# Performance work log

Measured on AMD Instinct MI355X. Metric: run time of the kernel, lower is better.

## Reference

```python
import jax, jax.numpy as jnp
import numpy as np

NB_STEPS = 50
ALPHA = 0.9
NUM_RNN_STEPS = 2
B = 4096
NUM_FEATURE = 100
IN_D = 5
HIDDEN = [64, 64, 64]
P1 = (1.1, 1.1, 1.5, 2.0, 2.5)   # IntegrandNN_outer_level powers
P2 = (1.5, 2.0, 2.5, 3.0, 3.5)   # IntegrandNN powers


def _cc(nb_steps):
    # Clenshaw-Curtis weights/steps, identical to UMNN's compute_cc_weights
    n = nb_steps
    i = np.arange(n + 1, dtype=np.float64).reshape(-1, 1)
    lam = np.cos(i @ i.T * np.pi / n)
    lam[:, 0] = 0.5
    lam[:, -1] *= 0.5
    lam = lam * 2.0 / n
    W = np.zeros(n + 1)
    even = np.arange(0, n + 1, 2)
    W[even] = 2.0 / (1.0 - even.astype(np.float64) ** 2)
    W[0] = 1.0
    ccw = (lam.T @ W).astype(np.float32)                         # [n+1]
    steps = np.cos(np.arange(n + 1) * np.pi / n).astype(np.float32)  # [n+1]
    return jnp.asarray(ccw), jnp.asarray(steps)

CC_W, CC_S = _cc(NB_STEPS)


def _mlp(xh, Ws, bs):
    # Linear+ReLU stack with ELU on the last layer (ReLU popped, ELU appended)
    h = xh
    for W, b in zip(Ws[:-1], bs[:-1]):
        h = jax.nn.relu(h @ W.T + b)
    return jax.nn.elu(h @ Ws[-1].T + bs[-1])


def _integrand(x, h, Ws, bs, Wf, powers):
    z = _mlp(jnp.concatenate([x, h], axis=1), Ws, bs) + 1.0      # [N,1], z >= 0
    feats = jnp.concatenate([z ** p for p in powers], axis=1)    # [N,5]
    return jax.nn.relu((1.0 / (feats + 1.0)) @ Wf.T)             # [N,1]


def _integrate(x0, xT, h, f):
    # ParallelNeuralIntegral forward: CC quadrature of f from x0 to xT
    Bn, S = x0.shape[0], NB_STEPS + 1
    X = x0[:, None, :] + (xT - x0)[:, None, :] * (CC_S[None, :, None] + 1.0) / 2.0  # [B,S,1]
    hs = jnp.broadcast_to(h[:, None, :], (Bn, S, h.shape[1])).reshape(-1, h.shape[1])
    dz = f(X.reshape(-1, 1), hs).reshape(Bn, S, 1)
    return (dz * CC_W[None, :, None]).sum(1) * (xT - x0) / 2.0   # [B,1]


def setup_inputs() -> dict:
    key = jax.random.key(0)
    ks = jax.random.split(key, 24)
    def lin(k, o, i):
        return jax.random.normal(k, (o, i), jnp.float32) / np.sqrt(i)
    d = {}
    d["x_"] = jax.random.normal(ks[0], (B, NUM_FEATURE), jnp.float32)
    d["h_"] = jax.random.normal(ks[1], (B, IN_D - 1), jnp.float32)
    d["log_weight"] = jnp.ones((1, NUM_FEATURE), jnp.float32)     # reset_parameters -> 1
    d["sigmoid_param"] = jnp.zeros((1,), jnp.float32)
    sizes = [IN_D] + HIDDEN + [1]
    for tag, base in (("f1", 2), ("f2", 12)):
        for li, (i, o) in enumerate(zip(sizes[:-1], sizes[1:])):
            d[f"{tag}_W{li}"] = lin(ks[base + 2 * li], o, i)
            d[f"{tag}_b{li}"] = jnp.zeros((o,), jnp.float32)
        d[f"{tag}_Wf"] = jnp.abs(lin(ks[base + 9], 1, 5))         # reset_params -> abs
    return d


def reference(x_, h_, log_weight, sigmoid_param,
              f1_W0, f1_b0, f1_W1, f1_b1, f1_W2, f1_b2, f1_W3, f1_b3, f1_Wf,
              f2_W0, f2_b0, f2_W1, f2_b1, f2_W2, f2_b2, f2_W3, f2_b3, f2_Wf):
    f1Ws = [f1_W0, f1_W1, f1_W2, f1_W3]; f1bs = [f1_b0, f1_b1, f1_b2, f1_b3]
    f2Ws = [f2_W0, f2_W1, f2_W2, f2_W3]; f2bs = [f2_b0, f2_b1, f2_b2, f2_b3]
    f1 = lambda x, h: _integrand(x, h, f1Ws, f1bs, f1_Wf, P1)
    f2 = lambda x, h: _integrand(x, h, f2Ws, f2bs, f2_Wf, P2)

    # modular function: linear to [B,1] then sum over dim 1 -> [B,1]
    xm = jnp.sum(x_ * log_weight[0], axis=1, keepdims=True)
    lam = jax.nn.sigmoid(sigmoid_param[0])

    I1 = jnp.zeros_like(xm)
    I2 = jnp.zeros_like(xm)
    out_first = None
    for _ in range(NUM_RNN_STEPS):
        x = (1.0 - lam) * xm + lam * I1
        x2 = (1.0 - lam) * xm + lam * I2
        out_first = f1(x2, h_)
        I1 = _integrate(jnp.zeros_like(x), x, h_, f1)
        xmax = jnp.max(x2) + 10.0
        xfinal = jnp.zeros_like(x) + xmax
        I2 = (1.0 / ALPHA) * _integrate(x2, xfinal, h_, f2)
    return I1, out_first, I2
```

## Files before the change

### kernel.cpp

```cpp
#include <hip/hip_runtime.h>
#include <math.h>

typedef _Float16 half8v __attribute__((ext_vector_type(8)));
typedef _Float16 half4v __attribute__((ext_vector_type(4)));
typedef _Float16 half2v __attribute__((ext_vector_type(2)));
typedef float float4v __attribute__((ext_vector_type(4)));

#define BB    4096
#define NS    51
#define INV_ALPHA (1.0f/0.9f)

#define WS_CCW   0
#define WS_CCS   64
#define WS_LAM   128
#define WS_KEY64 160
#define WS_PM    256
#define WS_XM    512
#define WS_X     (WS_XM + BB)
#define WS_X2    (WS_X + BB)
#define WS_H     16384
#define H_NET    8192
#define H_W2     4096
#define H_W0     16384
#define H_W3     20480

#if defined(__has_builtin)
#if __has_builtin(__builtin_amdgcn_rcpf)
#define FRCP(x) __builtin_amdgcn_rcpf(x)
#endif
#if __has_builtin(__builtin_amdgcn_exp2f)
#define FEXP2(x) __builtin_amdgcn_exp2f(x)
#endif
#if __has_builtin(__builtin_amdgcn_logf)
#define FLOG2(x) __builtin_amdgcn_logf(x)
#endif
#endif
#ifndef FRCP
#define FRCP(x) (1.0f / (x))
#endif
#ifndef FEXP2
#define FEXP2(x) exp2f(x)
#endif
#ifndef FLOG2
#define FLOG2(x) log2f(x)
#endif

__device__ __forceinline__ unsigned fkey(float f) {
    int i = __float_as_int(f);
    return (i >= 0) ? ((unsigned)i + 0x80000000u) : ~(unsigned)i;
}
__device__ __forceinline__ float fkey_inv(unsigned k) {
    return (k & 0x80000000u) ? __int_as_float((int)(k - 0x80000000u))
                             : __int_as_float((int)~k);
}

__device__ __forceinline__ int swz(int row, int cb) {
    return (row << 6) + (((cb ^ (row & 7)) & 7) << 3);
}

__device__ __forceinline__ half4v pk_relu4(float4v c) {
#if defined(__has_builtin) && __has_builtin(__builtin_amdgcn_cvt_pkrtz)
    half2v a = __builtin_bit_cast(half2v,
        __builtin_amdgcn_cvt_pkrtz(fmaxf(c[0], 0.0f), fmaxf(c[1], 0.0f)));
    half2v b = __builtin_bit_cast(half2v,
        __builtin_amdgcn_cvt_pkrtz(fmaxf(c[2], 0.0f), fmaxf(c[3], 0.0f)));
    half4v o; o[0] = a[0]; o[1] = a[1]; o[2] = b[0]; o[3] = b[1];
    return o;
#else
    half4v o;
    o[0] = (_Float16)fmaxf(c[0], 0.0f); o[1] = (_Float16)fmaxf(c[1], 0.0f);
    o[2] = (_Float16)fmaxf(c[2], 0.0f); o[3] = (_Float16)fmaxf(c[3], 0.0f);
    return o;
#endif
}

__global__ void k_setup(const float* __restrict__ x_, const float* __restrict__ lw,
                        const float* __restrict__ sp,
                        const float* __restrict__ f1W0, const float* __restrict__ f1W1,
                        const float* __restrict__ f1W2, const float* __restrict__ f1W3,
                        const float* __restrict__ f2W0, const float* __restrict__ f2W1,
                        const float* __restrict__ f2W2, const float* __restrict__ f2W3,
                        float* __restrict__ ws) {
    _Float16* wh = (_Float16*)(ws + WS_H);
    const int blk = blockIdx.x, tid = threadIdx.x;
    if (blk < 256) {
        int wave = tid >> 6, lane = tid & 63;
        float vmax = -1e30f;
        for (int r = 0; r < 4; ++r) {
            int row = blk * 16 + wave * 4 + r;
            float v = 0.0f;
            for (int i = lane; i < 100; i += 64) v = fmaf(x_[row * 100 + i], lw[i], v);
            #pragma unroll
            for (int off = 32; off > 0; off >>= 1) v += __shfl_xor(v, off, 64);
            if (lane == 0) ws[WS_XM + row] = v;
            vmax = fmaxf(vmax, v);
        }
        __shared__ float sm[4];
        if (lane == 0) sm[wave] = vmax;
        __syncthreads();
        if (tid == 0)
            ws[WS_PM + blk] = fmaxf(fmaxf(sm[0], sm[1]), fmaxf(sm[2], sm[3]));
    } else if (blk < 272) {
        int t = (blk - 256) * 256 + tid;
        wh[t]                = (_Float16)f1W1[t];
        wh[H_W2 + t]         = (_Float16)f1W2[t];
        wh[H_NET + t]        = (_Float16)f2W1[t];
        wh[H_NET + H_W2 + t] = (_Float16)f2W2[t];
        if (t < 2048) {
            int j = t >> 5, k = t & 31;
            wh[H_W0 + t]        = (k < 5) ? (_Float16)f1W0[j * 5 + k] : (_Float16)0.0f;
            wh[H_W0 + 2048 + t] = (k < 5) ? (_Float16)f2W0[j * 5 + k] : (_Float16)0.0f;
        }
        if (t < 64) {
            wh[H_W3 + t]      = (_Float16)f1W3[t];
            wh[H_W3 + 64 + t] = (_Float16)f2W3[t];
        }
    } else {
        if (tid < 64) ((unsigned*)ws)[WS_KEY64 + tid] = 0u;
        if (tid == 64) ws[WS_LAM] = 1.0f / (1.0f + expf(-sp[0]));
        if (tid >= 128 && tid <= 178) {
            int s = tid - 128;
            ws[WS_CCS + s] = cospif((float)s / 50.0f);
            float acc = 0.0f;
            for (int a = 0; a <= 50; ++a) {
                float w;
                if (a == 0) w = 1.0f;
                else if ((a & 1) == 0) w = 2.0f / (1.0f - (float)(a * a));
                else continue;
                float l;
                if (s == 0) l = 0.5f;
                else {
                    int m = (a * s) % 100;
                    l = cospif((float)m / 50.0f);
                    if (s == 50) l *= 0.5f;
                }
                acc += l * 0.04f * w;
            }
            ws[WS_CCW + s] = acc;
        }
    }
}

__global__ __launch_bounds__(64, 2) void k_int(
    int mode, float* __restrict__ ws, const float* __restrict__ h_,
    const float* __restrict__ f1b0, const float* __restrict__ f1b1,
    const float* __restrict__ f1b2, const float* __restrict__ f1b3,
    const float* __restrict__ f1Wf,
    const float* __restrict__ f2b0, const float* __restrict__ f2b1,
    const float* __restrict__ f2b2, const float* __restrict__ f2b3,
    const float* __restrict__ f2Wf,
    float* __restrict__ out)
{
    __shared__ _Float16 act[64 * 64];

    const int blk = blockIdx.x;
    const int lane = threadIdx.x;
    const int lo = lane & 15, q = lane >> 4;

    const float* xm = ws + WS_XM;
    const float* xarr = ws + WS_X;
    const float* x2arr = ws + WS_X2;
    const _Float16* wh = (const _Float16*)(ws + WS_H);
    const float lam = ws[WS_LAM];
    const float oml = 1.0f - lam;

    const bool u2 = (blk >= 1024);
    const int kb0 = u2 ? blk - 1024 : blk;

    const _Float16* W0h = wh + H_W0 + (u2 ? 2048 : 0);
    const _Float16* W1h = wh + (u2 ? H_NET : 0);
    const _Float16* W2h = W1h + H_W2;
    const _Float16* W3h = wh + H_W3 + (u2 ? 64 : 0);
    const float* B0 = u2 ? f2b0 : f1b0;
    const float* B1 = u2 ? f2b1 : f1b1;
    const float* B2 = u2 ? f2b2 : f1b2;
    const float* B3 = u2 ? f2b3 : f1b3;
    const float* WF = u2 ? f2Wf : f1Wf;
    const float p0 = u2 ? 1.5f : 1.1f;
    const float p1 = u2 ? 2.0f : 1.1f;
    const float p2 = u2 ? 2.5f : 1.5f;
    const float p3 = u2 ? 3.0f : 2.0f;
    const float p4 = u2 ? 3.5f : 2.5f;

    half8v A0w[4], A1w[4][2], A2w[4][2];
    float4v b0r[4], b1r[4], b2r[4];
    half4v w3r[4];
    #pragma unroll
    for (int m = 0; m < 4; ++m) {
        A0w[m]    = *(const half8v*)(W0h + (16 * m + lo) * 32 + q * 8);
        A1w[m][0] = *(const half8v*)(W1h + (16 * m + lo) * 64 + q * 8);
        A1w[m][1] = *(const half8v*)(W1h + (16 * m + lo) * 64 + 32 + q * 8);
        A2w[m][0] = *(const half8v*)(W2h + (16 * m + lo) * 64 + q * 8);
        A2w[m][1] = *(const half8v*)(W2h + (16 * m + lo) * 64 + 32 + q * 8);
        b0r[m] = *(const float4v*)(B0 + 16 * m + q * 4);
        b1r[m] = *(const float4v*)(B1 + 16 * m + q * 4);
        b2r[m] = *(const float4v*)(B2 + 16 * m + q * 4);
        w3r[m] = *(const half4v*)(W3h + 16 * m + 4 * q);
    }
    const float B3s = B3[0];
    const float wf0 = WF[0], wf1 = WF[1], wf2 = WF[2], wf3 = WF[3], wf4 = WF[4];

    float t_r[4];
    #pragma unroll
    for (int n = 0; n < 4; ++n) {
        int r = 16 * n + lo;
        t_r[n] = (ws[WS_CCS + (r > 50 ? 50 : r)] + 1.0f) * 0.5f;
    }
    const float ccw_l = (lane <= 50) ? ws[WS_CCW + lane] : 0.0f;

    float xmax = 0.0f;
    if (u2) {
        if (mode) {
            float v = fkey_inv(((const unsigned*)ws)[WS_KEY64 + lane]);
            #pragma unroll
            for (int off = 32; off > 0; off >>= 1) v = fmaxf(v, __shfl_xor(v, off, 64));
            xmax = v + 10.0f;
        } else {
            const float* pm = ws + WS_PM;
            float v = fmaxf(fmaxf(pm[lane], pm[lane + 64]),
                            fmaxf(pm[lane + 128], pm[lane + 192]));
            #pragma unroll
            for (int off = 32; off > 0; off >>= 1) v = fmaxf(v, __shfl_xor(v, off, 64));
            xmax = oml * v + 10.0f;
        }
    }

    const int nitems = (mode && !u2 && blk < 64) ? 5 : 4;

    #pragma clang loop unroll(disable)
    for (int it = 0; it < nitems; ++it) {
        const bool last = (it == 4);
        int b = kb0 + 1024 * it;
        float xb = 0.0f, x0 = 0.0f;
        float4 h4u = {0, 0, 0, 0};

        half8v Bf0[4];
        if (last) {
            int b0i = blk * 64;
            #pragma unroll
            for (int n = 0; n < 4; ++n) {
                int idx = b0i + 16 * n + lo;
                float xr = x2arr[idx];
                float4 hr = ((const float4*)h_)[idx];
                half8v e;
                e[0] = (_Float16)xr; e[1] = (_Float16)hr.x; e[2] = (_Float16)hr.y;
                e[3] = (_Float16)hr.z; e[4] = (_Float16)hr.w;
                e[5] = (_Float16)0.0f; e[6] = (_Float16)0.0f; e[7] = (_Float16)0.0f;
                half8v z;
                #pragma unroll
                for (int t2 = 0; t2 < 8; ++t2) z[t2] = (_Float16)0.0f;
                Bf0[n] = (q == 0) ? e : z;
            }
        } else {
            if (!u2) xb = mode ? xarr[b] : oml * xm[b];
            else     x0 = mode ? x2arr[b] : oml * xm[b];
            h4u = ((const float4*)h_)[b];
            #pragma unroll
            for (int n = 0; n < 4; ++n) {
                float xr = (!u2) ? xb * t_r[n] : x0 + (xmax - x0) * t_r[n];
                half8v e;
                e[0] = (_Float16)xr; e[1] = (_Float16)h4u.x; e[2] = (_Float16)h4u.y;
                e[3] = (_Float16)h4u.z; e[4] = (_Float16)h4u.w;
                e[5] = (_Float16)0.0f; e[6] = (_Float16)0.0f; e[7] = (_Float16)0.0f;
                half8v z;
                #pragma unroll
                for (int t2 = 0; t2 < 8; ++t2) z[t2] = (_Float16)0.0f;
                Bf0[n] = (q == 0) ? e : z;
            }
        }

        #pragma unroll
        for (int m = 0; m < 4; ++m)
            #pragma unroll
            for (int n = 0; n < 4; ++n) {
                float4v c = __builtin_amdgcn_mfma_f32_16x16x32_f16(A0w[m], Bf0[n], b0r[m], 0, 0, 0);
                *(half4v*)(act + swz(16 * n + lo, 2 * m + (q >> 1)) + 4 * (q & 1)) = pk_relu4(c);
            }

        {
            half8v Bf[2][4];
            #pragma unroll
            for (int kb = 0; kb < 2; ++kb)
                #pragma unroll
                for (int n = 0; n < 4; ++n)
                    Bf[kb][n] = *(const half8v*)(act + swz(16 * n + lo, 4 * kb + q));
            #pragma unroll
            for (int m = 0; m < 4; ++m)
                #pragma unroll
                for (int n = 0; n < 4; ++n) {
                    float4v c = __builtin_amdgcn_mfma_f32_16x16x32_f16(A1w[m][0], Bf[0][n], b1r[m], 0, 0, 0);
                    c = __builtin_amdgcn_mfma_f32_16x16x32_f16(A1w[m][1], Bf[1][n], c, 0, 0, 0);
                    *(half4v*)(act + swz(16 * n + lo, 2 * m + (q >> 1)) + 4 * (q & 1)) = pk_relu4(c);
                }
        }

        float part[4] = {0.0f, 0.0f, 0.0f, 0.0f};
        {
            half8v Bf[2][4];
            #pragma unroll
            for (int kb = 0; kb < 2; ++kb)
                #pragma unroll
                for (int n = 0; n < 4; ++n)
                    Bf[kb][n] = *(const half8v*)(act + swz(16 * n + lo, 4 * kb + q));
            #pragma unroll
            for (int m = 0; m < 4; ++m)
                #pragma unroll
                for (int n = 0; n < 4; ++n) {
                    float4v c = __builtin_amdgcn_mfma_f32_16x16x32_f16(A2w[m][0], Bf[0][n], b2r[m], 0, 0, 0);
                    c = __builtin_amdgcn_mfma_f32_16x16x32_f16(A2w[m][1], Bf[1][n], c, 0, 0, 0);
                    #pragma unroll
                    for (int e = 0; e < 4; ++e)
                        part[n] = fmaf((float)w3r[m][e], fmaxf(c[e], 0.0f), part[n]);
                }
        }

        #pragma unroll
        for (int n = 0; n < 4; ++n) {
            part[n] += __shfl_xor(part[n], 16, 64);
            part[n] += __shfl_xor(part[n], 32, 64);
        }
        float y = B3s + (q == 0 ? part[0] : q == 1 ? part[1] : q == 2 ? part[2] : part[3]);

        if (y <= 0.0f) y = FEXP2(y * 1.44269504f) - 1.0f;
        float z = y + 1.0f;
        float lg = FLOG2(z);
        float g = wf0 * FRCP(FEXP2(p0 * lg) + 1.0f)
                + wf1 * FRCP(FEXP2(p1 * lg) + 1.0f)
                + wf2 * FRCP(FEXP2(p2 * lg) + 1.0f)
                + wf3 * FRCP(FEXP2(p3 * lg) + 1.0f)
                + wf4 * FRCP(FEXP2(p4 * lg) + 1.0f);
        float val = fmaxf(g, 0.0f);

        if (last) {
            out[BB + blk * 64 + lane] = val;
            continue;
        }

        float c = ccw_l * val;
        #pragma unroll
        for (int off = 32; off > 0; off >>= 1) c += __shfl_xor(c, off, 64);

        if (lane == 0) {
            if (!u2) {
                float I1 = c * xb * 0.5f;
                out[b] = I1;
                if (!mode) ws[WS_X + b] = oml * xm[b] + lam * I1;
            } else {
                float I2 = c * (xmax - x0) * 0.5f * INV_ALPHA;
                out[2 * BB + b] = I2;
                if (!mode) {
                    float x2n = oml * xm[b] + lam * I2;
                    ws[WS_X2 + b] = x2n;
                    atomicMax((unsigned*)ws + WS_KEY64 + (b & 63), fkey(x2n));
                }
            }
        }
    }
}

extern "C" void kernel_launch(void* const* d_in, const int* in_sizes, int n_in,
                              void* d_out, int out_size, void* d_ws, size_t ws_size,
                              hipStream_t stream) {
    const float* x_  = (const float*)d_in[0];
    const float* h_  = (const float*)d_in[1];
    const float* lw  = (const float*)d_in[2];
    const float* sp  = (const float*)d_in[3];
    const float* f1W0 = (const float*)d_in[4];   const float* f1b0 = (const float*)d_in[5];
    const float* f1W1 = (const float*)d_in[6];   const float* f1b1 = (const float*)d_in[7];
    const float* f1W2 = (const float*)d_in[8];   const float* f1b2 = (const float*)d_in[9];
    const float* f1W3 = (const float*)d_in[10];  const float* f1b3 = (const float*)d_in[11];
    const float* f1Wf = (const float*)d_in[12];
    const float* f2W0 = (const float*)d_in[13];  const float* f2b0 = (const float*)d_in[14];
    const float* f2W1 = (const float*)d_in[15];  const float* f2b1 = (const float*)d_in[16];
    const float* f2W2 = (const float*)d_in[17];  const float* f2b2 = (const float*)d_in[18];
    const float* f2W3 = (const float*)d_in[19];  const float* f2b3 = (const float*)d_in[20];
    const float* f2Wf = (const float*)d_in[21];
    float* out = (float*)d_out;
    float* ws  = (float*)d_ws;

    k_setup<<<273, 256, 0, stream>>>(x_, lw, sp,
                                     f1W0, f1W1, f1W2, f1W3,
                                     f2W0, f2W1, f2W2, f2W3, ws);
    k_int<<<2048, 64, 0, stream>>>(0, ws, h_,
        f1b0, f1b1, f1b2, f1b3, f1Wf, f2b0, f2b1, f2b2, f2b3, f2Wf, out);
    k_int<<<2048, 64, 0, stream>>>(1, ws, h_,
        f1b0, f1b1, f1b2, f1b3, f1Wf, f2b0, f2b1, f2b2, f2b3, f2Wf, out);
}
```

Before: 144.9 us.

## Remap quadrature tiles to batch-major and accumulate partial integrals via atomics

Each wave now handles 64 batch rows at 3-4 quadrature nodes and accumulates weighted partial sums per row with atomicAdd. Previously a wave handled one batch row across all 51 nodes and ran a cross-lane shuffle reduction. The x/x2 recurrence and the global max are moved into a small k_pre kernel using a block reduction, which replaces the per-element atomicMax key scheme. Output zeroing moves into setup, and the out_first pass becomes extra blocks. The change removes the wave-wide shuffle reduction and padded lanes (51 of 64 used). It adds an extra launch, many atomics, and nondeterministic summation order.

```diff
diff --git a/kernel.cpp b/kernel.cpp
--- a/kernel.cpp
+++ b/kernel.cpp
@@ -7,22 +7,21 @@
 typedef float float4v __attribute__((ext_vector_type(4)));
 
 #define BB    4096
-#define NS    51
 #define INV_ALPHA (1.0f/0.9f)
 
-#define WS_CCW   0
-#define WS_CCS   64
-#define WS_LAM   128
-#define WS_KEY64 160
-#define WS_PM    256
-#define WS_XM    512
-#define WS_X     (WS_XM + BB)
-#define WS_X2    (WS_X + BB)
-#define WS_H     16384
-#define H_NET    8192
-#define H_W2     4096
-#define H_W0     16384
-#define H_W3     20480
+#define WS_CCW  0
+#define WS_CCS  64
+#define WS_LAM  128
+#define WS_PM16 160
+#define WS_PM   256
+#define WS_XM   512
+#define WS_X    (WS_XM + BB)
+#define WS_X2   (WS_X + BB)
+#define WS_H    16384
+#define H_NET   8192
+#define H_W2    4096
+#define H_W0    16384
+#define H_W3    20480
 
 #if defined(__has_builtin)
 #if __has_builtin(__builtin_amdgcn_rcpf)
@@ -44,15 +43,6 @@
 #ifndef FLOG2
 #define FLOG2(x) log2f(x)
 #endif
-
-__device__ __forceinline__ unsigned fkey(float f) {
-    int i = __float_as_int(f);
-    return (i >= 0) ? ((unsigned)i + 0x80000000u) : ~(unsigned)i;
-}
-__device__ __forceinline__ float fkey_inv(unsigned k) {
-    return (k & 0x80000000u) ? __int_as_float((int)(k - 0x80000000u))
-                             : __int_as_float((int)~k);
-}
 
 __device__ __forceinline__ int swz(int row, int cb) {
     return (row << 6) + (((cb ^ (row & 7)) & 7) << 3);
@@ -80,7 +70,7 @@
                         const float* __restrict__ f1W2, const float* __restrict__ f1W3,
                         const float* __restrict__ f2W0, const float* __restrict__ f2W1,
                         const float* __restrict__ f2W2, const float* __restrict__ f2W3,
-                        float* __restrict__ ws) {
+                        float* __restrict__ ws, float* __restrict__ out) {
     _Float16* wh = (_Float16*)(ws + WS_H);
     const int blk = blockIdx.x, tid = threadIdx.x;
     if (blk < 256) {
@@ -115,11 +105,10 @@
             wh[H_W3 + t]      = (_Float16)f1W3[t];
             wh[H_W3 + 64 + t] = (_Float16)f2W3[t];
         }
-    } else {
-        if (tid < 64) ((unsigned*)ws)[WS_KEY64 + tid] = 0u;
+    } else if (blk == 272) {
         if (tid == 64) ws[WS_LAM] = 1.0f / (1.0f + expf(-sp[0]));
-        if (tid >= 128 && tid <= 178) {
-            int s = tid - 128;
+        if (tid <= 50) {
+            int s = tid;
             ws[WS_CCS + s] = cospif((float)s / 50.0f);
             float acc = 0.0f;
             for (int a = 0; a <= 50; ++a) {
@@ -138,7 +127,32 @@
             }
             ws[WS_CCW + s] = acc;
         }
-    }
+    } else {
+        int t = (blk - 273) * 256 + tid;
+        out[t < BB ? t : BB + t] = 0.0f;
+    }
+}
+
+__global__ void k_pre(float* __restrict__ ws, float* __restrict__ out) {
+    int b = blockIdx.x * 256 + threadIdx.x;
+    float lam = ws[WS_LAM];
+    float m = ws[WS_XM + b];
+    float xv  = (1.0f - lam) * m + lam * out[b];
+    float x2v = (1.0f - lam) * m + lam * out[2 * BB + b];
+    ws[WS_X + b] = xv;
+    ws[WS_X2 + b] = x2v;
+    out[b] = 0.0f;
+    out[2 * BB + b] = 0.0f;
+    __shared__ float red[256];
+    red[threadIdx.x] = x2v;
+    __syncthreads();
+    #pragma unroll
+    for (int off = 128; off > 0; off >>= 1) {
+        if (threadIdx.x < off)
+            red[threadIdx.x] = fmaxf(red[threadIdx.x], red[threadIdx.x + off]);
+        __syncthreads();
+    }
+    if (threadIdx.x == 0) ws[WS_PM16 + blockIdx.x] = red[0];
 }
 
 __global__ __launch_bounds__(64, 2) void k_int(
@@ -164,8 +178,18 @@
     const float lam = ws[WS_LAM];
     const float oml = 1.0f - lam;
 
-    const bool u2 = (blk >= 1024);
-    const int kb0 = u2 ? blk - 1024 : blk;
+    const bool is_of = (blk >= 2048);
+    int base, w = 0, np;
+    bool u2;
+    if (is_of) {
+        base = (blk - 2048) << 6; u2 = false; np = 1;
+    } else {
+        int g = blk >> 4;
+        w = blk & 15;
+        u2 = (g >= 64);
+        base = (g & 63) << 6;
+        np = (w < 3) ? 4 : 3;
+    }
 
     const _Float16* W0h = wh + H_W0 + (u2 ? 2048 : 0);
     const _Float16* W1h = wh + (u2 ? H_NET : 0);
@@ -200,18 +224,23 @@
     const float B3s = B3[0];
     const float wf0 = WF[0], wf1 = WF[1], wf2 = WF[2], wf3 = WF[3], wf4 = WF[4];
 
-    float t_r[4];
+    float xr_r[4];
+    float4 h4r[4];
     #pragma unroll
     for (int n = 0; n < 4; ++n) {
-        int r = 16 * n + lo;
-        t_r[n] = (ws[WS_CCS + (r > 50 ? 50 : r)] + 1.0f) * 0.5f;
-    }
-    const float ccw_l = (lane <= 50) ? ws[WS_CCW + lane] : 0.0f;
+        int idx = base + 16 * n + lo;
+        float v;
+        if (is_of)      v = x2arr[idx];
+        else if (mode)  v = u2 ? x2arr[idx] : xarr[idx];
+        else            v = oml * xm[idx];
+        xr_r[n] = v;
+        h4r[n] = ((const float4*)h_)[idx];
+    }
 
     float xmax = 0.0f;
     if (u2) {
         if (mode) {
-            float v = fkey_inv(((const unsigned*)ws)[WS_KEY64 + lane]);
+            float v = (lane < 16) ? ws[WS_PM16 + lane] : -1e30f;
             #pragma unroll
             for (int off = 32; off > 0; off >>= 1) v = fmaxf(v, __shfl_xor(v, off, 64));
             xmax = v + 10.0f;
@@ -225,48 +254,32 @@
         }
     }
 
-    const int nitems = (mode && !u2 && blk < 64) ? 5 : 4;
+    float acc = 0.0f;
 
     #pragma clang loop unroll(disable)
-    for (int it = 0; it < nitems; ++it) {
-        const bool last = (it == 4);
-        int b = kb0 + 1024 * it;
-        float xb = 0.0f, x0 = 0.0f;
-        float4 h4u = {0, 0, 0, 0};
+    for (int p = 0; p < np; ++p) {
+        const int s = w + 16 * p;
+        float t = 0.0f, ccw_s = 0.0f;
+        if (!is_of) {
+            t = (ws[WS_CCS + s] + 1.0f) * 0.5f;
+            ccw_s = ws[WS_CCW + s];
+        }
 
         half8v Bf0[4];
-        if (last) {
-            int b0i = blk * 64;
-            #pragma unroll
-            for (int n = 0; n < 4; ++n) {
-                int idx = b0i + 16 * n + lo;
-                float xr = x2arr[idx];
-                float4 hr = ((const float4*)h_)[idx];
-                half8v e;
-                e[0] = (_Float16)xr; e[1] = (_Float16)hr.x; e[2] = (_Float16)hr.y;
-                e[3] = (_Float16)hr.z; e[4] = (_Float16)hr.w;
-                e[5] = (_Float16)0.0f; e[6] = (_Float16)0.0f; e[7] = (_Float16)0.0f;
-                half8v z;
-                #pragma unroll
-                for (int t2 = 0; t2 < 8; ++t2) z[t2] = (_Float16)0.0f;
-                Bf0[n] = (q == 0) ? e : z;
-            }
-        } else {
-            if (!u2) xb = mode ? xarr[b] : oml * xm[b];
-            else     x0 = mode ? x2arr[b] : oml * xm[b];
-            h4u = ((const float4*)h_)[b];
-            #pragma unroll
-            for (int n = 0; n < 4; ++n) {
-                float xr = (!u2) ? xb * t_r[n] : x0 + (xmax - x0) * t_r[n];
-                half8v e;
-                e[0] = (_Float16)xr; e[1] = (_Float16)h4u.x; e[2] = (_Float16)h4u.y;
-                e[3] = (_Float16)h4u.z; e[4] = (_Float16)h4u.w;
-                e[5] = (_Float16)0.0f; e[6] = (_Float16)0.0f; e[7] = (_Float16)0.0f;
-                half8v z;
-                #pragma unroll
-                for (int t2 = 0; t2 < 8; ++t2) z[t2] = (_Float16)0.0f;
-                Bf0[n] = (q == 0) ? e : z;
-            }
+        #pragma unroll
+        for (int n = 0; n < 4; ++n) {
+            float xin;
+            if (is_of)   xin = xr_r[n];
+            else if (u2) xin = fmaf(t, xmax - xr_r[n], xr_r[n]);
+            else         xin = xr_r[n] * t;
+            half8v e;
+            e[0] = (_Float16)xin; e[1] = (_Float16)h4r[n].x; e[2] = (_Float16)h4r[n].y;
+            e[3] = (_Float16)h4r[n].z; e[4] = (_Float16)h4r[n].w;
+            e[5] = (_Float16)0.0f; e[6] = (_Float16)0.0f; e[7] = (_Float16)0.0f;
+            half8v z;
+            #pragma unroll
+            for (int t2 = 0; t2 < 8; ++t2) z[t2] = (_Float16)0.0f;
+            Bf0[n] = (q == 0) ? e : z;
         }
 
         #pragma unroll
@@ -331,30 +344,15 @@
                 + wf4 * FRCP(FEXP2(p4 * lg) + 1.0f);
         float val = fmaxf(g, 0.0f);
 
-        if (last) {
-            out[BB + blk * 64 + lane] = val;
-            continue;
-        }
-
-        float c = ccw_l * val;
-        #pragma unroll
-        for (int off = 32; off > 0; off >>= 1) c += __shfl_xor(c, off, 64);
-
-        if (lane == 0) {
-            if (!u2) {
-                float I1 = c * xb * 0.5f;
-                out[b] = I1;
-                if (!mode) ws[WS_X + b] = oml * xm[b] + lam * I1;
-            } else {
-                float I2 = c * (xmax - x0) * 0.5f * INV_ALPHA;
-                out[2 * BB + b] = I2;
-                if (!mode) {
-                    float x2n = oml * xm[b] + lam * I2;
-                    ws[WS_X2 + b] = x2n;
-                    atomicMax((unsigned*)ws + WS_KEY64 + (b & 63), fkey(x2n));
-                }
-            }
-        }
+        if (is_of) { out[BB + base + lane] = val; return; }
+        acc += ccw_s * val;
+    }
+
+    const float x_l = (q == 0 ? xr_r[0] : q == 1 ? xr_r[1] : q == 2 ? xr_r[2] : xr_r[3]);
+    if (!u2) {
+        atomicAdd(out + base + lane, acc * x_l * 0.5f);
+    } else {
+        atomicAdd(out + 2 * BB + base + lane, acc * (xmax - x_l) * 0.5f * INV_ALPHA);
     }
 }
 
@@ -378,11 +376,12 @@
     float* out = (float*)d_out;
     float* ws  = (float*)d_ws;
 
-    k_setup<<<273, 256, 0, stream>>>(x_, lw, sp,
+    k_setup<<<305, 256, 0, stream>>>(x_, lw, sp,
                                      f1W0, f1W1, f1W2, f1W3,
-                                     f2W0, f2W1, f2W2, f2W3, ws);
+                                     f2W0, f2W1, f2W2, f2W3, ws, out);
     k_int<<<2048, 64, 0, stream>>>(0, ws, h_,
         f1b0, f1b1, f1b2, f1b3, f1Wf, f2b0, f2b1, f2b2, f2b3, f2Wf, out);
-    k_int<<<2048, 64, 0, stream>>>(1, ws, h_,
+    k_pre<<<16, 256, 0, stream>>>(ws, out);
+    k_int<<<2112, 64, 0, stream>>>(1, ws, h_,
         f1b0, f1b1, f1b2, f1b3, f1Wf, f2b0, f2b1, f2b2, f2b3, f2Wf, out);
 }
```

Result: no change. 144.0 us (median of 2 runs) (-0.6%).
